# Performance work log

Hardware: AMD Instinct MI355X
Metric: run time of the kernel (lower is better)

## Reference

```python
import jax, jax.numpy as jnp
import numpy as np

K_STEPS = 10
ALPHA = 0.1


def setup_inputs() -> dict:
    key = jax.random.key(0)
    k0, k1, k2, k3 = jax.random.split(key, 4)
    N, E, C_IN, C_HID, C_OUT = 100000, 3200000, 512, 256, 64
    x = jax.random.normal(k0, (N, C_IN), dtype=jnp.float32)
    edge_index = jax.random.randint(k1, (2, E), 0, N, dtype=jnp.int64)
    W1 = jax.random.normal(k2, (C_IN, C_HID), dtype=jnp.float32) * (1.0 / np.sqrt(C_IN))
    b1 = jnp.zeros((C_HID,), dtype=jnp.float32)
    W2 = jax.random.normal(k3, (C_HID, C_OUT), dtype=jnp.float32) * (1.0 / np.sqrt(C_HID))
    b2 = jnp.zeros((C_OUT,), dtype=jnp.float32)
    return {"x": x, "edge_index": edge_index, "W1": W1, "b1": b1, "W2": W2, "b2": b2}


def reference(x, edge_index, W1, b1, W2, b2):
    N = x.shape[0]
    src, dst = edge_index[0], edge_index[1]
    # add self-loops (PyG APPNP default)
    loop = jnp.arange(N, dtype=src.dtype)
    src = jnp.concatenate([src, loop])
    dst = jnp.concatenate([dst, loop])
    # GCN symmetric normalization: D^{-1/2} A D^{-1/2}
    deg = jax.ops.segment_sum(jnp.ones_like(dst, dtype=x.dtype), dst, num_segments=N)
    dinv = jnp.where(deg > 0, deg ** -0.5, jnp.zeros_like(deg))
    norm = dinv[src] * dinv[dst]  # [E+N]
    # MLP (dropout is identity at inference)
    h = jax.nn.relu(x @ W1 + b1) @ W2 + b2  # [N, C_OUT]
    # K-step APPNP propagation with teleport
    out = h
    for _ in range(K_STEPS):
        msg = norm[:, None] * out[src]  # [E+N, C_OUT]
        agg = jax.ops.segment_sum(msg, dst, num_segments=N)
        out = (1.0 - ALPHA) * agg + ALPHA * h
    return jax.nn.log_softmax(out, axis=1)
```

## Files before the change

kernel.cpp:

```cpp
#include <hip/hip_runtime.h>
#include <hip/hip_bf16.h>

#define C_IN  512
#define C_HID 256
#define C_OUT 64
#define K_STEPS 10
#define ALPHA 0.1f

#define BKT_SHIFT 9
#define BKT_NODES 512
#define BCAP 24576
#define EPB 4096

typedef _Float16 half8 __attribute__((ext_vector_type(8)));
typedef float f32x4 __attribute__((ext_vector_type(4)));


__global__ __launch_bounds__(256) void k_bucketA(
    const int* __restrict__ src, const int* __restrict__ dst, int E,
    int* __restrict__ bcursor, long long* __restrict__ bedges, int nbkt)
{
    __shared__ int lcount[256];
    __shared__ int lbase[256];
    int t = threadIdx.x;
    int base = blockIdx.x * EPB;
    for (int i = t; i < nbkt; i += 256) lcount[i] = 0;
    __syncthreads();

    int       mybkt[16];
    int       myoff[16];
    long long mypk[16];
    #pragma unroll
    for (int j = 0; j < 16; j++) {
        int e = base + j * 256 + t;
        if (e < E) {
            int s = src[e], d = dst[e];
            int b = d >> BKT_SHIFT;
            mybkt[j] = b;
            mypk[j]  = ((long long)d << 32) | (unsigned int)s;
            myoff[j] = atomicAdd(&lcount[b], 1);
        } else {
            mybkt[j] = -1;
        }
    }
    __syncthreads();
    for (int i = t; i < nbkt; i += 256)
        lbase[i] = lcount[i] ? atomicAdd(&bcursor[i], lcount[i]) : 0;
    __syncthreads();
    #pragma unroll
    for (int j = 0; j < 16; j++) {
        if (mybkt[j] >= 0) {
            int p = lbase[mybkt[j]] + myoff[j];
            bedges[(size_t)mybkt[j] * BCAP + p] = mypk[j];
        }
    }
}

__global__ void k_bscan(const int* __restrict__ bcursor, int nbkt,
                        int* __restrict__ bktbase, int* __restrict__ rowptr,
                        int N, int E)
{
    if (blockIdx.x == 0 && threadIdx.x == 0) {
        int run = 0;
        for (int i = 0; i < nbkt; i++) { bktbase[i] = run; run += bcursor[i]; }
        rowptr[N] = E;
    }
}

__global__ __launch_bounds__(256) void k_bfin(
    const int* __restrict__ bcursor, const int* __restrict__ bktbase,
    const long long* __restrict__ bedges, int* __restrict__ rowptr,
    float* __restrict__ dinv, int* __restrict__ csr_src, int N)
{
    __shared__ int lcnt[BKT_NODES];
    __shared__ int lofs[BKT_NODES];
    __shared__ int sdata[256];
    int b = blockIdx.x, t = threadIdx.x;
    int nodebase = b << BKT_SHIFT;

    lcnt[2 * t] = 0; lcnt[2 * t + 1] = 0;
    __syncthreads();

    int cnt = bcursor[b];
    const long long* be = bedges + (size_t)b * BCAP;
    for (int i = t; i < cnt; i += 256) {
        int d = (int)(be[i] >> 32);
        atomicAdd(&lcnt[d - nodebase], 1);
    }
    __syncthreads();

    int v0 = lcnt[2 * t], v1 = lcnt[2 * t + 1];
    int psum = v0 + v1;
    sdata[t] = psum;
    __syncthreads();
    for (int off = 1; off < 256; off <<= 1) {
        int y = 0;
        if (t >= off) y = sdata[t - off];
        __syncthreads();
        sdata[t] += y;
        __syncthreads();
    }
    int excl = sdata[t] - psum;
    int base = bktbase[b];
    lofs[2 * t]     = base + excl;
    lofs[2 * t + 1] = base + excl + v0;
    __syncthreads();

    #pragma unroll
    for (int j = 0; j < 2; j++) {
        int i = 2 * t + j;
        int node = nodebase + i;
        if (node < N) {
            rowptr[node] = lofs[i];
            dinv[node] = 1.0f / sqrtf((float)(lcnt[i] + 1));
        }
    }
    __syncthreads();

    for (int i = t; i < cnt; i += 256) {
        long long pk = be[i];
        int d = (int)(pk >> 32);
        int s = (int)pk;
        int p = atomicAdd(&lofs[d - nodebase], 1);
        csr_src[p] = s;
    }
}


__global__ void k_wt(const float* __restrict__ W1, const float* __restrict__ W2,
                     _Float16* __restrict__ W1t, _Float16* __restrict__ W2t)
{
    int i = blockIdx.x * 256 + threadIdx.x;
    if (i < C_IN * C_HID) {
        int k = i >> 8, n = i & 255;
        W1t[(size_t)n * 512 + k] = (_Float16)W1[i];
    } else {
        int j = i - C_IN * C_HID;
        if (j < C_HID * C_OUT) {
            int k = j >> 6, n = j & 63;
            W2t[(size_t)n * 256 + k] = (_Float16)W2[j];
        }
    }
}


__global__ __launch_bounds__(256, 2) void k_mlp1(
    const float* __restrict__ A, const _Float16* __restrict__ Bt,
    const float* __restrict__ bias, _Float16* __restrict__ C, int M)
{
    __shared__ float lds[2][128 * 32];

    int t    = threadIdx.x;
    int lane = t & 63;
    int wid  = t >> 6;
    int bm   = blockIdx.x * 128;
    int wr   = wid >> 1;
    int wc   = wid & 1;
    int mrow = lane & 15;
    int kg   = lane >> 4;

    int srow = wid * 8 + (lane >> 3);
    int cgs  = (lane & 7) ^ (lane >> 3);

    const float* gsrc[4];
    #pragma unroll
    for (int q = 0; q < 4; q++) {
        int gr = bm + q * 32 + srow;
        if (gr >= M) gr = M - 1;
        gsrc[q] = A + (size_t)gr * 512 + cgs * 4;
    }

    #define STAGE(buf, ks)                                                       \
        {                                                                        \
            _Pragma("unroll")                                                    \
            for (int q = 0; q < 4; q++) {                                        \
                __builtin_amdgcn_global_load_lds(                                \
                    (const __attribute__((address_space(1))) void*)(gsrc[q] + (ks) * 32), \
                    (__attribute__((address_space(3))) void*)((char*)&lds[buf][0] + q * 4096 + wid * 1024), \
                    16, 0, 0);                                                   \
            }                                                                    \
        }

    f32x4 acc[4][8] = {};

    int m7 = lane & 7;
    int rbase[4];
    #pragma unroll
    for (int mi = 0; mi < 4; mi++)
        rbase[mi] = (wr * 64 + mi * 16 + mrow) * 32;
    int p0 = ((2 * kg) ^ m7) * 4;
    int p1 = ((2 * kg + 1) ^ m7) * 4;

    STAGE(0, 0);
    __syncthreads();

    int cur = 0;
    for (int ks = 0; ks < 16; ks++) {
        if (ks < 15) STAGE(cur ^ 1, ks + 1);

        half8 b[8];
        #pragma unroll
        for (int ni = 0; ni < 8; ni++) {
            int n = wc * 128 + ni * 16 + mrow;
            b[ni] = *(const half8*)(Bt + (size_t)n * 512 + ks * 32 + kg * 8);
        }

        half8 a[4];
        #pragma unroll
        for (int mi = 0; mi < 4; mi++) {
            f32x4 lo = *(const f32x4*)&lds[cur][rbase[mi] + p0];
            f32x4 hi = *(const f32x4*)&lds[cur][rbase[mi] + p1];
            a[mi][0] = (_Float16)lo[0]; a[mi][1] = (_Float16)lo[1];
            a[mi][2] = (_Float16)lo[2]; a[mi][3] = (_Float16)lo[3];
            a[mi][4] = (_Float16)hi[0]; a[mi][5] = (_Float16)hi[1];
            a[mi][6] = (_Float16)hi[2]; a[mi][7] = (_Float16)hi[3];
        }

        #pragma unroll
        for (int mi = 0; mi < 4; mi++)
            #pragma unroll
            for (int ni = 0; ni < 8; ni++)
                acc[mi][ni] = __builtin_amdgcn_mfma_f32_16x16x32_f16(
                    a[mi], b[ni], acc[mi][ni], 0, 0, 0);

        __syncthreads();
        cur ^= 1;
    }
    #undef STAGE

    #pragma unroll
    for (int mi = 0; mi < 4; mi++) {
        #pragma unroll
        for (int ni = 0; ni < 8; ni++) {
            int n = wc * 128 + ni * 16 + mrow;
            float bv = bias[n];
            #pragma unroll
            for (int rg = 0; rg < 4; rg++) {
                int row = bm + wr * 64 + mi * 16 + kg * 4 + rg;
                if (row < M) {
                    float v = acc[mi][ni][rg] + bv;
                    C[(size_t)row * 256 + n] = (_Float16)fmaxf(v, 0.f);
                }
            }
        }
    }
}


__global__ __launch_bounds__(256) void k_mlp2(
    const _Float16* __restrict__ A, const _Float16* __restrict__ Bt,
    const float* __restrict__ bias, const float* __restrict__ dinv,
    _Float16* __restrict__ C, _Float16* __restrict__ Y, int M)
{
    int lane = threadIdx.x & 63;
    int wid  = threadIdx.x >> 6;
    int bm   = blockIdx.x * 256 + wid * 64;
    int mrow = lane & 15;
    int kg   = lane >> 4;
    f32x4 acc[4][4] = {};

    int r[4];
    #pragma unroll
    for (int mi = 0; mi < 4; mi++) {
        int rr = bm + mi * 16 + mrow;
        r[mi] = rr < M ? rr : M - 1;
    }

    for (int k0 = 0; k0 < 256; k0 += 32) {
        int k = k0 + kg * 8;
        half8 a[4], b[4];
        #pragma unroll
        for (int mi = 0; mi < 4; mi++)
            a[mi] = *(const half8*)(A + (size_t)r[mi] * 256 + k);
        #pragma unroll
        for (int ni = 0; ni < 4; ni++) {
            int n = ni * 16 + mrow;
            b[ni] = *(const half8*)(Bt + (size_t)n * 256 + k);
        }
        #pragma unroll
        for (int mi = 0; mi < 4; mi++)
            #pragma unroll
            for (int ni = 0; ni < 4; ni++)
                acc[mi][ni] = __builtin_amdgcn_mfma_f32_16x16x32_f16(
                    a[mi], b[ni], acc[mi][ni], 0, 0, 0);
    }

    #pragma unroll
    for (int mi = 0; mi < 4; mi++) {
        #pragma unroll
        for (int ni = 0; ni < 4; ni++) {
            int n = ni * 16 + mrow;
            float bv = bias[n];
            #pragma unroll
            for (int rg = 0; rg < 4; rg++) {
                int row = bm + mi * 16 + kg * 4 + rg;
                if (row < M) {
                    float v = acc[mi][ni][rg] + bv;
                    C[(size_t)row * 64 + n] = (_Float16)v;
                    Y[(size_t)row * 64 + n] = (_Float16)(v * dinv[row]);
                }
            }
        }
    }
}


template <bool LAST>
__global__ __launch_bounds__(256) void k_prop(
    const int* __restrict__ rowptr, const int* __restrict__ csr_src,
    const float* __restrict__ dinv, const _Float16* __restrict__ h,
    const _Float16* __restrict__ ycur, _Float16* __restrict__ ynxt,
    float* __restrict__ out, int N)
{
    int node = blockIdx.x * 4 + (threadIdx.x >> 6);
    if (node >= N) return;
    int lane = threadIdx.x & 63;
    int g  = lane >> 3;
    int cg = lane & 7;

    int beg = rowptr[node], end = rowptr[node + 1];
    float dn = dinv[node];
    half8 ys = *(const half8*)(ycur + ((size_t)node << 6) + cg * 8);
    half8 hv = *(const half8*)(h    + ((size_t)node << 6) + cg * 8);

    float acc[8] = {};
    for (int e = beg + g; e < end; e += 32) {
        int i1 = e + 8, i2 = e + 16, i3 = e + 24;
        float p1 = (i1 < end) ? 1.f : 0.f;
        float p2 = (i2 < end) ? 1.f : 0.f;
        float p3 = (i3 < end) ? 1.f : 0.f;
        int s0 = csr_src[e];
        int s1 = csr_src[(i1 < end) ? i1 : e];
        int s2 = csr_src[(i2 < end) ? i2 : e];
        int s3 = csr_src[(i3 < end) ? i3 : e];
        half8 v0 = *(const half8*)(ycur + ((size_t)s0 << 6) + cg * 8);
        half8 v1 = *(const half8*)(ycur + ((size_t)s1 << 6) + cg * 8);
        half8 v2 = *(const half8*)(ycur + ((size_t)s2 << 6) + cg * 8);
        half8 v3 = *(const half8*)(ycur + ((size_t)s3 << 6) + cg * 8);
        #pragma unroll
        for (int c = 0; c < 8; c++)
            acc[c] += ((float)v0[c] + p1 * (float)v1[c])
                    + (p2 * (float)v2[c] + p3 * (float)v3[c]);
    }

    #pragma unroll
    for (int c = 0; c < 8; c++) {
        float a = acc[c];
        a += __shfl_xor(a, 8);
        a += __shfl_xor(a, 16);
        a += __shfl_xor(a, 32);
        acc[c] = a;
    }

    float o[8];
    #pragma unroll
    for (int c = 0; c < 8; c++)
        o[c] = (1.0f - ALPHA) * dn * (acc[c] + (float)ys[c]) + ALPHA * (float)hv[c];

    if (!LAST) {
        if (g == 0) {
            half8 w;
            #pragma unroll
            for (int c = 0; c < 8; c++) w[c] = (_Float16)(dn * o[c]);
            *(half8*)(ynxt + ((size_t)node << 6) + cg * 8) = w;
        }
    } else {
        float m = o[0];
        #pragma unroll
        for (int c = 1; c < 8; c++) m = fmaxf(m, o[c]);
        m = fmaxf(m, __shfl_xor(m, 1));
        m = fmaxf(m, __shfl_xor(m, 2));
        m = fmaxf(m, __shfl_xor(m, 4));
        float s = 0.f;
        #pragma unroll
        for (int c = 0; c < 8; c++) s += __expf(o[c] - m);
        s += __shfl_xor(s, 1);
        s += __shfl_xor(s, 2);
        s += __shfl_xor(s, 4);
        float ls = m + logf(s);
        if (g == 0) {
            f32x4 w0, w1;
            #pragma unroll
            for (int c = 0; c < 4; c++) { w0[c] = o[c] - ls; w1[c] = o[c + 4] - ls; }
            float* p = out + ((size_t)node << 6) + cg * 8;
            *(f32x4*)p = w0;
            *(f32x4*)(p + 4) = w1;
        }
    }
}


extern "C" void kernel_launch(void* const* d_in, const int* in_sizes, int n_in,
                              void* d_out, int out_size, void* d_ws, size_t ws_size,
                              hipStream_t stream) {
    const float* x  = (const float*)d_in[0];
    const int*   ei = (const int*)d_in[1];
    const float* W1 = (const float*)d_in[2];
    const float* b1 = (const float*)d_in[3];
    const float* W2 = (const float*)d_in[4];
    const float* b2 = (const float*)d_in[5];

    const int N = in_sizes[0] / C_IN;
    const int E = in_sizes[1] / 2;
    const int* src = ei;
    const int* dst = ei + E;

    char* ws = (char*)d_ws;
    size_t off = 0;
    auto alloc = [&](size_t bytes) -> void* {
        void* p = ws + off;
        off += (bytes + 255) & ~(size_t)255;
        return p;
    };

    int nbkt = (N + BKT_NODES - 1) / BKT_NODES;

    int*       rowptr  = (int*)      alloc((size_t)4 * (N + 1));
    float*     dinv    = (float*)    alloc((size_t)4 * N);
    int*       bcursor = (int*)      alloc((size_t)4 * nbkt);
    int*       bktbase = (int*)      alloc((size_t)4 * (nbkt + 1));
    int*       csr_src = (int*)      alloc((size_t)4 * E);
    _Float16*  W1t     = (_Float16*) alloc((size_t)2 * C_IN * C_HID);
    _Float16*  W2t     = (_Float16*) alloc((size_t)2 * C_HID * C_OUT);
    _Float16*  hmid    = (_Float16*) alloc((size_t)2 * N * C_HID);
    _Float16*  h       = (_Float16*) alloc((size_t)2 * N * C_OUT);
    _Float16*  ybuf0   = (_Float16*) alloc((size_t)2 * N * C_OUT);
    _Float16*  ybuf1   = (_Float16*) alloc((size_t)2 * N * C_OUT);
    _Float16*  ybuf2   = (_Float16*) alloc((size_t)2 * N * C_OUT);

    long long* bedges = (long long*)hmid;

    hipMemsetAsync(bcursor, 0, (size_t)4 * nbkt, stream);
    k_bucketA<<<(E + EPB - 1) / EPB, 256, 0, stream>>>(src, dst, E, bcursor, bedges, nbkt);
    k_bscan<<<1, 64, 0, stream>>>(bcursor, nbkt, bktbase, rowptr, N, E);
    k_bfin<<<nbkt, 256, 0, stream>>>(bcursor, bktbase, bedges, rowptr, dinv, csr_src, N);

    int wtot = C_IN * C_HID + C_HID * C_OUT;
    k_wt<<<(wtot + 255) / 256, 256, 0, stream>>>(W1, W2, W1t, W2t);
    k_mlp1<<<(N + 127) / 128, 256, 0, stream>>>(x, W1t, b1, hmid, N);
    k_mlp2<<<(N + 255) / 256, 256, 0, stream>>>(hmid, W2t, b2, dinv, h, ybuf0, N);

    int pgrid = (N + 3) / 4;
    _Float16* ycur = ybuf0;
    for (int it = 0; it < K_STEPS - 1; ++it) {
        _Float16* ynxt = (it & 1) ? ybuf2 : ybuf1;
        k_prop<false><<<pgrid, 256, 0, stream>>>(rowptr, csr_src, dinv, h, ycur, ynxt, nullptr, N);
        ycur = ynxt;
    }
    k_prop<true><<<pgrid, 256, 0, stream>>>(rowptr, csr_src, dinv, h, ycur, nullptr, (float*)d_out, N);
}
```

Before: 758.8 us.

## Fuse the two MLP GEMMs, keeping the hidden tile in LDS

Merges k_mlp1 and k_mlp2 into one kernel. The ReLU hidden tile (128x256 fp16) is written to swizzled shared memory, and the second GEMM with W2 runs straight from LDS, so the 51MB hidden activation no longer makes a round trip through global memory. It needs 64KB of dynamic LDS per block, which may lower occupancy below the two blocks per CU the launch bounds ask for. The edge bucket buffer now gets its own workspace allocation instead of aliasing hmid.

```diff
diff --git a/kernel.cpp b/kernel.cpp
--- a/kernel.cpp
+++ b/kernel.cpp
@@ -144,11 +144,15 @@
 }
 
 
-__global__ __launch_bounds__(256, 2) void k_mlp1(
+__global__ __launch_bounds__(256, 2) void k_mlp(
     const float* __restrict__ A, const _Float16* __restrict__ Bt,
-    const float* __restrict__ bias, _Float16* __restrict__ C, int M)
-{
-    __shared__ float lds[2][128 * 32];
+    const _Float16* __restrict__ W2t, const float* __restrict__ bias1,
+    const float* __restrict__ bias2, const float* __restrict__ dinv,
+    _Float16* __restrict__ H, _Float16* __restrict__ Y, int M)
+{
+    extern __shared__ __align__(16) char smem[];
+    float*    stagef = (float*)smem;
+    _Float16* htile  = (_Float16*)smem;
 
     int t    = threadIdx.x;
     int lane = t & 63;
@@ -176,7 +180,7 @@
             for (int q = 0; q < 4; q++) {                                        \
                 __builtin_amdgcn_global_load_lds(                                \
                     (const __attribute__((address_space(1))) void*)(gsrc[q] + (ks) * 32), \
-                    (__attribute__((address_space(3))) void*)((char*)&lds[buf][0] + q * 4096 + wid * 1024), \
+                    (__attribute__((address_space(3))) void*)(smem + (buf) * 16384 + q * 4096 + wid * 1024), \
                     16, 0, 0);                                                   \
             }                                                                    \
         }
@@ -208,8 +212,8 @@
         half8 a[4];
         #pragma unroll
         for (int mi = 0; mi < 4; mi++) {
-            f32x4 lo = *(const f32x4*)&lds[cur][rbase[mi] + p0];
-            f32x4 hi = *(const f32x4*)&lds[cur][rbase[mi] + p1];
+            f32x4 lo = *(const f32x4*)&stagef[cur * 4096 + rbase[mi] + p0];
+            f32x4 hi = *(const f32x4*)&stagef[cur * 4096 + rbase[mi] + p1];
             a[mi][0] = (_Float16)lo[0]; a[mi][1] = (_Float16)lo[1];
             a[mi][2] = (_Float16)lo[2]; a[mi][3] = (_Float16)lo[3];
             a[mi][4] = (_Float16)hi[0]; a[mi][5] = (_Float16)hi[1];
@@ -232,72 +236,55 @@
     for (int mi = 0; mi < 4; mi++) {
         #pragma unroll
         for (int ni = 0; ni < 8; ni++) {
-            int n = wc * 128 + ni * 16 + mrow;
-            float bv = bias[n];
+            int col = wc * 128 + ni * 16 + mrow;
+            float bv = bias1[col];
+            int chunk = col >> 3, within = col & 7;
             #pragma unroll
             for (int rg = 0; rg < 4; rg++) {
-                int row = bm + wr * 64 + mi * 16 + kg * 4 + rg;
-                if (row < M) {
-                    float v = acc[mi][ni][rg] + bv;
-                    C[(size_t)row * 256 + n] = (_Float16)fmaxf(v, 0.f);
-                }
+                int row = wr * 64 + mi * 16 + kg * 4 + rg;
+                float v = fmaxf(acc[mi][ni][rg] + bv, 0.f);
+                htile[row * 256 + ((chunk ^ (row & 7)) << 3) + within] = (_Float16)v;
             }
         }
     }
-}
-
-
-__global__ __launch_bounds__(256) void k_mlp2(
-    const _Float16* __restrict__ A, const _Float16* __restrict__ Bt,
-    const float* __restrict__ bias, const float* __restrict__ dinv,
-    _Float16* __restrict__ C, _Float16* __restrict__ Y, int M)
-{
-    int lane = threadIdx.x & 63;
-    int wid  = threadIdx.x >> 6;
-    int bm   = blockIdx.x * 256 + wid * 64;
-    int mrow = lane & 15;
-    int kg   = lane >> 4;
-    f32x4 acc[4][4] = {};
-
-    int r[4];
-    #pragma unroll
-    for (int mi = 0; mi < 4; mi++) {
-        int rr = bm + mi * 16 + mrow;
-        r[mi] = rr < M ? rr : M - 1;
-    }
-
-    for (int k0 = 0; k0 < 256; k0 += 32) {
-        int k = k0 + kg * 8;
-        half8 a[4], b[4];
-        #pragma unroll
-        for (int mi = 0; mi < 4; mi++)
-            a[mi] = *(const half8*)(A + (size_t)r[mi] * 256 + k);
+    __syncthreads();
+
+    f32x4 acc2[2][4] = {};
+    for (int ks = 0; ks < 8; ks++) {
+        half8 b2[4];
         #pragma unroll
         for (int ni = 0; ni < 4; ni++) {
             int n = ni * 16 + mrow;
-            b[ni] = *(const half8*)(Bt + (size_t)n * 256 + k);
-        }
-        #pragma unroll
-        for (int mi = 0; mi < 4; mi++)
+            b2[ni] = *(const half8*)(W2t + (size_t)n * 256 + ks * 32 + kg * 8);
+        }
+        half8 a2[2];
+        #pragma unroll
+        for (int mi = 0; mi < 2; mi++) {
+            int row = wid * 32 + mi * 16 + mrow;
+            int chunk = ks * 4 + kg;
+            a2[mi] = *(const half8*)&htile[row * 256 + ((chunk ^ (row & 7)) << 3)];
+        }
+        #pragma unroll
+        for (int mi = 0; mi < 2; mi++)
             #pragma unroll
             for (int ni = 0; ni < 4; ni++)
-                acc[mi][ni] = __builtin_amdgcn_mfma_f32_16x16x32_f16(
-                    a[mi], b[ni], acc[mi][ni], 0, 0, 0);
-    }
-
-    #pragma unroll
-    for (int mi = 0; mi < 4; mi++) {
+                acc2[mi][ni] = __builtin_amdgcn_mfma_f32_16x16x32_f16(
+                    a2[mi], b2[ni], acc2[mi][ni], 0, 0, 0);
+    }
+
+    #pragma unroll
+    for (int mi = 0; mi < 2; mi++) {
         #pragma unroll
         for (int ni = 0; ni < 4; ni++) {
-            int n = ni * 16 + mrow;
-            float bv = bias[n];
+            int col = ni * 16 + mrow;
+            float bv = bias2[col];
             #pragma unroll
             for (int rg = 0; rg < 4; rg++) {
-                int row = bm + mi * 16 + kg * 4 + rg;
+                int row = bm + wid * 32 + mi * 16 + kg * 4 + rg;
                 if (row < M) {
-                    float v = acc[mi][ni][rg] + bv;
-                    C[(size_t)row * 64 + n] = (_Float16)v;
-                    Y[(size_t)row * 64 + n] = (_Float16)(v * dinv[row]);
+                    float v = acc2[mi][ni][rg] + bv;
+                    H[(size_t)row * 64 + col] = (_Float16)v;
+                    Y[(size_t)row * 64 + col] = (_Float16)(v * dinv[row]);
                 }
             }
         }
@@ -422,14 +409,12 @@
     int*       csr_src = (int*)      alloc((size_t)4 * E);
     _Float16*  W1t     = (_Float16*) alloc((size_t)2 * C_IN * C_HID);
     _Float16*  W2t     = (_Float16*) alloc((size_t)2 * C_HID * C_OUT);
-    _Float16*  hmid    = (_Float16*) alloc((size_t)2 * N * C_HID);
+    long long* bedges  = (long long*)alloc((size_t)8 * nbkt * BCAP);
     _Float16*  h       = (_Float16*) alloc((size_t)2 * N * C_OUT);
     _Float16*  ybuf0   = (_Float16*) alloc((size_t)2 * N * C_OUT);
     _Float16*  ybuf1   = (_Float16*) alloc((size_t)2 * N * C_OUT);
     _Float16*  ybuf2   = (_Float16*) alloc((size_t)2 * N * C_OUT);
 
-    long long* bedges = (long long*)hmid;
-
     hipMemsetAsync(bcursor, 0, (size_t)4 * nbkt, stream);
     k_bucketA<<<(E + EPB - 1) / EPB, 256, 0, stream>>>(src, dst, E, bcursor, bedges, nbkt);
     k_bscan<<<1, 64, 0, stream>>>(bcursor, nbkt, bktbase, rowptr, N, E);
@@ -437,8 +422,7 @@
 
     int wtot = C_IN * C_HID + C_HID * C_OUT;
     k_wt<<<(wtot + 255) / 256, 256, 0, stream>>>(W1, W2, W1t, W2t);
-    k_mlp1<<<(N + 127) / 128, 256, 0, stream>>>(x, W1t, b1, hmid, N);
-    k_mlp2<<<(N + 255) / 256, 256, 0, stream>>>(hmid, W2t, b2, dinv, h, ybuf0, N);
+    k_mlp<<<(N + 127) / 128, 256, 65536, stream>>>(x, W1t, W2t, b1, b2, dinv, h, ybuf0, N);
 
     int pgrid = (N + 3) / 4;
     _Float16* ycur = ybuf0;
```

Result: faster. 736.2 us (-3.0%).
